# Optimization experiments

Hardware: AMD Instinct MI355X
Metric: run time of the kernel (lower is better)

## Reference

```python
import jax, jax.numpy as jnp
import numpy as np

B, S, M, H, P, T = 32, 400, 400, 200, 16, 4

def setup_inputs() -> dict:
    key = jax.random.key(0)
    ks = jax.random.split(key, 20)
    sc = 0.05
    inp = {
        'att': jax.random.normal(ks[0], (B, S, M), jnp.float32),
        'mod': jax.random.normal(ks[1], (B, S, M), jnp.float32),
        'mask': jnp.ones((B, S), jnp.float32),
        # LSTMCell: input 2*M, hidden H, gate order i,f,g,o
        'lstm_Wih': jax.random.normal(ks[2], (4 * H, 2 * M), jnp.float32) * sc,
        'lstm_Whh': jax.random.normal(ks[3], (4 * H, H), jnp.float32) * sc,
        'lstm_bih': jnp.zeros((4 * H,), jnp.float32),
        'lstm_bhh': jnp.zeros((4 * H,), jnp.float32),
    }
    for pfx, off in (('s', 4), ('e', 11)):
        inp[pfx + '_rW'] = jax.random.normal(ks[off + 0], (H, 2 * M + H), jnp.float32) * sc
        inp[pfx + '_W1'] = jax.random.normal(ks[off + 1], (P * H, M + H), jnp.float32) * sc
        inp[pfx + '_b1'] = jnp.zeros((P * H,), jnp.float32)
        inp[pfx + '_W2'] = jax.random.normal(ks[off + 2], (P * H, H), jnp.float32) * sc
        inp[pfx + '_b2'] = jnp.zeros((P * H,), jnp.float32)
        inp[pfx + '_W3'] = jax.random.normal(ks[off + 3], (P, 2 * H), jnp.float32) * sc
        inp[pfx + '_b3'] = jnp.zeros((P,), jnp.float32)
    return inp

def _gather(mod, idx):
    # mod:[B,S,M], idx:[B] -> [B,M]
    return jnp.take_along_axis(mod, idx[:, None, None], axis=1)[:, 0, :]

def _lstm_cell(x, h, c, Wih, Whh, bih, bhh):
    g = x @ Wih.T + bih + h @ Whh.T + bhh  # [B,4H]
    i, f, gg, o = jnp.split(g, 4, axis=1)
    c2 = jax.nn.sigmoid(f) * c + jax.nn.sigmoid(i) * jnp.tanh(gg)
    h2 = jax.nn.sigmoid(o) * jnp.tanh(c2)
    return h2, c2

def _hmn(mod, h, us, ue, mask, rW, W1, b1, W2, b2, W3, b3):
    r = jnp.tanh(jnp.concatenate([h, us, ue], 1) @ rW.T)  # [B,H]
    x = jnp.concatenate([mod, jnp.broadcast_to(r[:, None, :], (B, S, H))], 2)  # [B,S,M+H]
    m1 = (x @ W1.T + b1).reshape(B, S, P, H).max(2)   # maxout 1
    m2 = (m1 @ W2.T + b2).reshape(B, S, P, H).max(2)  # maxout 2
    logits = (jnp.concatenate([m1, m2], 2) @ W3.T + b3).max(2)  # [B,S]
    logits = jnp.where(mask > 0, logits, -1e30)
    return jax.nn.log_softmax(logits, axis=1)

def reference(att, mod, mask, lstm_Wih, lstm_Whh, lstm_bih, lstm_bhh,
              s_rW, s_W1, s_b1, s_W2, s_b2, s_W3, s_b3,
              e_rW, e_W1, e_b1, e_W2, e_b2, e_W3, e_b3):
    s_prev = jnp.zeros((B,), jnp.int32)
    e_prev = jnp.sum(mask, 1).astype(jnp.int32) - 1
    h = jnp.zeros((B, H), mod.dtype)
    c = jnp.zeros((B, H), mod.dtype)
    log_p1s, log_p2s = [], []
    for _ in range(T):
        u_s = _gather(mod, s_prev)
        u_e = _gather(mod, e_prev)
        h, c = _lstm_cell(jnp.concatenate([u_s, u_e], 1), h, c,
                          lstm_Wih, lstm_Whh, lstm_bih, lstm_bhh)
        lp1 = _hmn(mod, h, u_s, u_e, mask, s_rW, s_W1, s_b1, s_W2, s_b2, s_W3, s_b3)
        s_prev = jnp.argmax(lp1, axis=1).astype(jnp.int32)
        u_s = _gather(mod, s_prev)
        lp2 = _hmn(mod, h, u_s, u_e, mask, e_rW, e_W1, e_b1, e_W2, e_b2, e_W3, e_b3)
        e_prev = jnp.argmax(lp2, axis=1).astype(jnp.int32)
        log_p1s.append(lp1)
        log_p2s.append(lp2)
    return jnp.stack(log_p1s, 1), jnp.stack(log_p2s, 1)  # each [B,T,S]
```

## Files before the change

kernel.cpp:

```cpp
#include <hip/hip_runtime.h>
#include <math.h>

#define NB 32
#define NS 400
#define NM 400
#define NH 200
#define NP 16
#define NT 4
#define NBS (NB*NS)
#define NPH (NP*NH)
#define NPH2 3328
#define NJT 13
#define NX  (2*NM)
#define NG  (4*NH)
#define NR  (2*NM+NH)
#define K1  1216
#define K2  608

typedef __attribute__((ext_vector_type(8))) short short8v;
typedef __attribute__((ext_vector_type(4))) float f32x4;
typedef __attribute__((ext_vector_type(4))) unsigned short us4;
typedef unsigned short ushort;

__device__ __forceinline__ float sigf(float x){ return 1.0f/(1.0f+expf(-x)); }

__device__ __forceinline__ ushort f2bf(float x){
  union{float f; unsigned u;} v; v.f=x;
  unsigned r = v.u + 0x7fffu + ((v.u>>16)&1u);
  return (ushort)(r>>16);
}
__device__ __forceinline__ float bf2f(ushort u){
  union{float f; unsigned v;} x; x.v = ((unsigned)u)<<16; return x.f;
}
__device__ __forceinline__ float wave_sum(float v){
  #pragma unroll
  for (int o=32;o>0;o>>=1) v += __shfl_xor(v, o);
  return v;
}

__global__ __launch_bounds__(256) void init_kernel(const float* __restrict__ mask,
    float* __restrict__ h, float* __restrict__ c,
    int* __restrict__ sprev, int* __restrict__ eprev){
  int b = blockIdx.x, tid = threadIdx.x;
  __shared__ float red[256];
  float s = 0.f;
  for (int i=tid;i<NS;i+=256) s += mask[(size_t)b*NS+i];
  red[tid]=s; __syncthreads();
  for (int st=128;st>0;st>>=1){ if(tid<st) red[tid]+=red[tid+st]; __syncthreads(); }
  if (tid==0){ sprev[b]=0; eprev[b]=(int)red[0]-1; }
  for (int i=tid;i<NH;i+=256){ h[(size_t)b*NH+i]=0.f; c[(size_t)b*NH+i]=0.f; }
}

__global__ __launch_bounds__(256) void conv_mod_k(const float* __restrict__ in, ushort* __restrict__ out){
  for (size_t i = (size_t)blockIdx.x*256+threadIdx.x; i < (size_t)NBS*K1; i += (size_t)gridDim.x*256){
    int r = (int)(i/K1), k = (int)(i%K1);
    ushort v = 0;
    if (k < 3*NM){
      float x = in[(size_t)r*NM + (k % NM)];
      ushort h = f2bf(x);
      v = (k < NM || k >= 2*NM) ? h : f2bf(x - bf2f(h));
    }
    out[i] = v;
  }
}
__global__ __launch_bounds__(256) void conv_w1_k(const float* __restrict__ in, ushort* __restrict__ out){
  for (size_t i = (size_t)blockIdx.x*256+threadIdx.x; i < (size_t)NPH2*K1; i += (size_t)gridDim.x*256){
    int jp = (int)(i/K1), k = (int)(i%K1);
    ushort v = 0;
    if (jp < NPH && k < 3*NM){
      int j = (jp&15)*NH + (jp>>4);
      float x = in[(size_t)j*(NM+NH) + (k % NM)];
      ushort h = f2bf(x);
      v = (k < 2*NM) ? h : f2bf(x - bf2f(h));
    }
    out[i] = v;
  }
}
__global__ __launch_bounds__(256) void conv_w2_k(const float* __restrict__ in, ushort* __restrict__ out){
  for (size_t i = (size_t)blockIdx.x*256+threadIdx.x; i < (size_t)NPH2*K2; i += (size_t)gridDim.x*256){
    int jp = (int)(i/K2), k = (int)(i%K2);
    ushort v = 0;
    if (jp < NPH && k < 3*NH){
      int j = (jp&15)*NH + (jp>>4);
      float x = in[(size_t)j*NH + (k % NH)];
      ushort h = f2bf(x);
      v = (k < 2*NH) ? h : f2bf(x - bf2f(h));
    }
    out[i] = v;
  }
}
__global__ __launch_bounds__(256) void conv_w1r_k(const float* __restrict__ in, float* __restrict__ out){
  for (size_t i = (size_t)blockIdx.x*256+threadIdx.x; i < (size_t)NH*NPH; i += (size_t)gridDim.x*256){
    int k = (int)(i/NPH), jp = (int)(i%NPH);
    int hh = jp>>4, p = jp&15, j = p*NH + hh;
    out[i] = in[(size_t)j*(NM+NH) + NM + k];
  }
}
__global__ __launch_bounds__(256) void permv_k(const float* __restrict__ in, float* __restrict__ out){
  int i = blockIdx.x*256+threadIdx.x;
  if (i < NPH) out[(i%NH)*NP + i/NH] = in[i];
  else if (i < NPH2) out[i] = 0.f;
}
__global__ __launch_bounds__(256) void pad_zero_k(ushort* __restrict__ p, int stride, int start, int width, int rows){
  for (size_t i = (size_t)blockIdx.x*256+threadIdx.x; i < (size_t)rows*width; i += (size_t)gridDim.x*256){
    int r = (int)(i/width), j = (int)(i%width);
    p[(size_t)r*stride + start + j] = 0;
  }
}

__global__ __launch_bounds__(256) void lstm_gates(const float* __restrict__ mod,
    const int* __restrict__ sprev, const int* __restrict__ eprev,
    const float* __restrict__ h,
    const float* __restrict__ Wih, const float* __restrict__ Whh,
    const float* __restrict__ bih, const float* __restrict__ bhh,
    float* __restrict__ gs){
  int b=blockIdx.x, tid=threadIdx.x;
  __shared__ float xs[NX+NH];
  const float* us = mod + ((size_t)b*NS + sprev[b])*NM;
  const float* ue = mod + ((size_t)b*NS + eprev[b])*NM;
  for (int i=tid;i<NM;i+=256){ xs[i]=us[i]; xs[NM+i]=ue[i]; }
  for (int i=tid;i<NH;i+=256) xs[NX+i]=h[(size_t)b*NH+i];
  __syncthreads();
  int w=tid>>6, lane=tid&63;
  int j = blockIdx.y*4 + w;
  const float* wih = Wih + (size_t)j*NX;
  const float* whh = Whh + (size_t)j*NH;
  float acc=0.f;
  for (int k=lane;k<NX;k+=64) acc += xs[k]*wih[k];
  for (int k=lane;k<NH;k+=64) acc += xs[NX+k]*whh[k];
  acc = wave_sum(acc);
  if (lane==0) gs[(size_t)b*NG+j] = acc + bih[j] + bhh[j];
}
__global__ __launch_bounds__(256) void lstm_update(const float* __restrict__ gs,
    float* __restrict__ h, float* __restrict__ c){
  int b=blockIdx.x, j=threadIdx.x;
  if (j<NH){
    float iv=gs[(size_t)b*NG+j], fv=gs[(size_t)b*NG+NH+j];
    float gv=gs[(size_t)b*NG+2*NH+j], ov=gs[(size_t)b*NG+3*NH+j];
    float c2 = sigf(fv)*c[(size_t)b*NH+j] + sigf(iv)*tanhf(gv);
    c[(size_t)b*NH+j]=c2;
    h[(size_t)b*NH+j]=sigf(ov)*tanhf(c2);
  }
}

__global__ __launch_bounds__(256) void r_kernel(const float* __restrict__ mod,
    const int* __restrict__ sprev, const int* __restrict__ eprev,
    const float* __restrict__ h, const float* __restrict__ rW,
    float* __restrict__ rbuf){
  int b=blockIdx.x, tid=threadIdx.x;
  __shared__ float zs[NR];
  const float* us = mod + ((size_t)b*NS + sprev[b])*NM;
  const float* ue = mod + ((size_t)b*NS + eprev[b])*NM;
  for (int i=tid;i<NH;i+=256) zs[i]=h[(size_t)b*NH+i];
  for (int i=tid;i<NM;i+=256){ zs[NH+i]=us[i]; zs[NH+NM+i]=ue[i]; }
  __syncthreads();
  int w=tid>>6, lane=tid&63;
  int j = blockIdx.y*4 + w;
  const float* wr = rW + (size_t)j*NR;
  float acc=0.f;
  for (int k=lane;k<NR;k+=64) acc += zs[k]*wr[k];
  acc = wave_sum(acc);
  if (lane==0) rbuf[(size_t)b*NH+j] = tanhf(acc);
}

__global__ __launch_bounds__(256) void prer_kernel(const float* __restrict__ rbuf,
    const float* __restrict__ W1rT, const float* __restrict__ b1p,
    float* __restrict__ prer){
  int b=blockIdx.x, tid=threadIdx.x;
  __shared__ float rs[NH];
  if (tid < NH) rs[tid] = rbuf[(size_t)b*NH+tid];
  __syncthreads();
  int jp = blockIdx.y*256 + tid;
  if (jp < NPH2){
    float acc = 0.f;
    if (jp < NPH){
      acc = b1p[jp];
      #pragma unroll 8
      for (int k=0;k<NH;k++) acc += rs[k]*W1rT[(size_t)k*NPH + jp];
    }
    prer[(size_t)b*NPH2 + jp] = acc;
  }
}

template<int MODE>
__global__ __launch_bounds__(512, 2) void gemm_fused(
    const ushort* __restrict__ A, const ushort* __restrict__ W,
    const float* __restrict__ bias, void* __restrict__ outp){
  constexpr int LDK = (MODE==1) ? K2 : K1;
  constexpr int NTI = LDK/32;
  __shared__ __align__(16) ushort As[4][256*32];
  __shared__ __align__(16) ushort Bs[4][256*32];
  __shared__ float biasLds[2][256];
  __shared__ float outT[256][16];
  const int tid = threadIdx.x;
  const int nwg = gridDim.x;
  const int q = nwg >> 3, r = nwg & 7;
  const int xcd = blockIdx.x & 7, sub = blockIdx.x >> 3;
  const int wkid = (xcd < r) ? (xcd*(q+1) + sub) : (r*(q+1) + (xcd-r)*q + sub);
  const int i0 = (wkid / NJT) * 256, j0 = (wkid % NJT) * 256;
  const int b0 = i0/NS;
  if (MODE==0){
    if (tid<256) biasLds[0][tid] = bias[(size_t)b0*NPH2 + j0 + tid];
    else { int b1r=(i0+255)/NS; biasLds[1][tid-256] = bias[(size_t)b1r*NPH2 + j0 + (tid-256)]; }
  } else {
    if (tid<256) biasLds[0][tid] = bias[j0+tid];
  }
  const int w = tid>>6, l = tid&63;
  const int wr = w>>2, wc = w&3;
  const int fr = l&15, fk = l>>4;
  const int srow = w*32 + (l>>2);
  const int sslot = l&3;
  const int swzc = (sslot ^ ((srow>>1)&3))*8;
  const ushort* gA0 = A + (size_t)(i0+srow)*LDK + swzc;
  const ushort* gB0 = W + (size_t)(j0+srow)*LDK + swzc;
  const int ldsOff = srow*32 + sslot*8;
  auto stage = [&](int slot, int kt){
    const ushort* a = gA0 + kt*32;
    const ushort* b = gB0 + kt*32;
    __builtin_amdgcn_global_load_lds((const __attribute__((address_space(1))) void*)a,
        (__attribute__((address_space(3))) void*)(&As[slot][ldsOff]), 16, 0, 0);
    __builtin_amdgcn_global_load_lds((const __attribute__((address_space(1))) void*)(a + 16*LDK),
        (__attribute__((address_space(3))) void*)(&As[slot][ldsOff + 16*32]), 16, 0, 0);
    __builtin_amdgcn_global_load_lds((const __attribute__((address_space(1))) void*)b,
        (__attribute__((address_space(3))) void*)(&Bs[slot][ldsOff]), 16, 0, 0);
    __builtin_amdgcn_global_load_lds((const __attribute__((address_space(1))) void*)(b + 16*LDK),
        (__attribute__((address_space(3))) void*)(&Bs[slot][ldsOff + 16*32]), 16, 0, 0);
  };
  f32x4 acc[8][4] = {};
  stage(0,0); stage(1,1); stage(2,2);
  for (int t=0; t<NTI; t++){
    if (t+2 < NTI)      asm volatile("s_waitcnt vmcnt(8)\n\ts_barrier" ::: "memory");
    else if (t+1 < NTI) asm volatile("s_waitcnt vmcnt(4)\n\ts_barrier" ::: "memory");
    else                asm volatile("s_waitcnt vmcnt(0)\n\ts_barrier" ::: "memory");
    const int s = t&3;
    short8v a[8], b[4];
    #pragma unroll
    for (int m=0;m<8;m++){
      int row = wr*128 + m*16 + fr;
      a[m] = *(const short8v*)&As[s][row*32 + ((fk ^ ((row>>1)&3))*8)];
    }
    #pragma unroll
    for (int n=0;n<4;n++){
      int row = wc*64 + n*16 + fr;
      b[n] = *(const short8v*)&Bs[s][row*32 + ((fk ^ ((row>>1)&3))*8)];
    }
    if (t+3 < NTI) stage((t+3)&3, t+3);
    __builtin_amdgcn_s_setprio(1);
    #pragma unroll
    for (int m=0;m<8;m++)
      #pragma unroll
      for (int n=0;n<4;n++)
        acc[m][n] = __builtin_amdgcn_mfma_f32_16x16x32_bf16(a[m], b[n], acc[m][n], 0,0,0);
    __builtin_amdgcn_s_setprio(0);
  }
  __syncthreads();
  const int blim = (b0+1)*NS;
  #pragma unroll
  for (int m=0;m<8;m++){
    #pragma unroll
    for (int n=0;n<4;n++){
      int colL = wc*64 + n*16 + fr;
      int rbase = wr*128 + m*16 + fk*4;
      #pragma unroll
      for (int reg=0; reg<4; reg++){
        int rowL = rbase + reg;
        float bv = (MODE==0 && (i0+rowL) >= blim) ? biasLds[1][colL] : biasLds[0][colL];
        float v = acc[m][n][reg] + bv;
        v = fmaxf(v, __shfl_xor(v,1));
        v = fmaxf(v, __shfl_xor(v,2));
        v = fmaxf(v, __shfl_xor(v,4));
        v = fmaxf(v, __shfl_xor(v,8));
        if (fr==0) outT[rowL][wc*4+n] = v;
      }
    }
  }
  __syncthreads();
  {
    int rowL = tid>>1;
    int hloc0 = (tid&1)*8;
    int hg0 = (j0>>4) + hloc0;
    if (hg0 < NH){
      int absrow = i0 + rowL;
      float v[8];
      #pragma unroll
      for (int qq=0;qq<8;qq++) v[qq] = outT[rowL][hloc0+qq];
      if (MODE==0){
        ushort* o = (ushort*)outp + (size_t)absrow*K2 + hg0;
        ushort hi[8], lo[8];
        #pragma unroll
        for (int qq=0;qq<8;qq++){ hi[qq]=f2bf(v[qq]); lo[qq]=f2bf(v[qq]-bf2f(hi[qq])); }
        *(us4*)(o)        = (us4){hi[0],hi[1],hi[2],hi[3]};
        *(us4*)(o+4)      = (us4){hi[4],hi[5],hi[6],hi[7]};
        *(us4*)(o+NH)     = (us4){lo[0],lo[1],lo[2],lo[3]};
        *(us4*)(o+NH+4)   = (us4){lo[4],lo[5],lo[6],lo[7]};
        *(us4*)(o+2*NH)   = (us4){hi[0],hi[1],hi[2],hi[3]};
        *(us4*)(o+2*NH+4) = (us4){hi[4],hi[5],hi[6],hi[7]};
      } else {
        float* o = (float*)outp + (size_t)absrow*NH + hg0;
        *(f32x4*)o     = (f32x4){v[0],v[1],v[2],v[3]};
        *(f32x4*)(o+4) = (f32x4){v[4],v[5],v[6],v[7]};
      }
    }
  }
}

__global__ __launch_bounds__(256) void logits_main(const ushort* __restrict__ m1e,
    const float* __restrict__ m2, const float* __restrict__ W3, const float* __restrict__ b3,
    const float* __restrict__ mask, float* __restrict__ lg){
  int b=blockIdx.x;
  int s=blockIdx.y*256+threadIdx.x;
  if (s >= NS) return;
  const ushort* a = m1e + (size_t)(b*NS+s)*K2;
  const float4* d = (const float4*)(m2 + (size_t)(b*NS+s)*NH);
  float acc[NP];
  #pragma unroll
  for (int p=0;p<NP;p++) acc[p]=b3[p];
  for (int k=0;k<NH/4;k++){
    us4 hv = *(const us4*)(a + 4*k);
    us4 lv = *(const us4*)(a + NH + 4*k);
    float4 dv = d[k];
    float a0=bf2f(hv.x)+bf2f(lv.x), a1=bf2f(hv.y)+bf2f(lv.y);
    float a2=bf2f(hv.z)+bf2f(lv.z), a3=bf2f(hv.w)+bf2f(lv.w);
    #pragma unroll
    for (int p=0;p<NP;p++){
      const float* wp = W3 + p*(2*NH) + 4*k;
      acc[p] += a0*wp[0]+a1*wp[1]+a2*wp[2]+a3*wp[3];
      const float* w2 = wp + NH;
      acc[p] += dv.x*w2[0]+dv.y*w2[1]+dv.z*w2[2]+dv.w*w2[3];
    }
  }
  float best=acc[0];
  #pragma unroll
  for (int p=1;p<NP;p++) best=fmaxf(best,acc[p]);
  lg[(size_t)b*NS+s] = (mask[(size_t)b*NS+s] > 0.f) ? best : -1e30f;
}

__global__ __launch_bounds__(256) void logits_fin(const float* __restrict__ lg,
    float* __restrict__ out, int t, int* __restrict__ prevIdx){
  int b=blockIdx.x, tid=threadIdx.x;
  __shared__ float rv[256]; __shared__ int ri[256]; __shared__ float sv[256];
  float bv=-INFINITY; int bi=NS;
  for (int s=tid;s<NS;s+=256){ float v=lg[(size_t)b*NS+s]; if (v>bv){bv=v;bi=s;} }
  rv[tid]=bv; ri[tid]=bi; __syncthreads();
  for (int st=128;st>0;st>>=1){
    if (tid<st){
      float v2=rv[tid+st]; int i2=ri[tid+st];
      if (v2>rv[tid] || (v2==rv[tid] && i2<ri[tid])){ rv[tid]=v2; ri[tid]=i2; }
    }
    __syncthreads();
  }
  float mx = rv[0];
  float ps=0.f;
  for (int s=tid;s<NS;s+=256) ps += expf(lg[(size_t)b*NS+s]-mx);
  sv[tid]=ps; __syncthreads();
  for (int st=128;st>0;st>>=1){ if (tid<st) sv[tid]+=sv[tid+st]; __syncthreads(); }
  float lse = mx + logf(sv[0]);
  for (int s=tid;s<NS;s+=256) out[((size_t)b*NT + t)*NS + s] = lg[(size_t)b*NS+s]-lse;
  if (tid==0) prevIdx[b]=ri[0];
}

extern "C" void kernel_launch(void* const* d_in, const int* in_sizes, int n_in,
                              void* d_out, int out_size, void* d_ws, size_t ws_size,
                              hipStream_t stream){
  const float* mod  = (const float*)d_in[1];
  const float* mask = (const float*)d_in[2];
  const float* Wih  = (const float*)d_in[3];
  const float* Whh  = (const float*)d_in[4];
  const float* bih  = (const float*)d_in[5];
  const float* bhh  = (const float*)d_in[6];
  const float* rW[2] = {(const float*)d_in[7],  (const float*)d_in[14]};
  const float* W1[2] = {(const float*)d_in[8],  (const float*)d_in[15]};
  const float* b1[2] = {(const float*)d_in[9],  (const float*)d_in[16]};
  const float* W2[2] = {(const float*)d_in[10], (const float*)d_in[17]};
  const float* b2[2] = {(const float*)d_in[11], (const float*)d_in[18]};
  const float* W3[2] = {(const float*)d_in[12], (const float*)d_in[19]};
  const float* b3[2] = {(const float*)d_in[13], (const float*)d_in[20]};
  float* out[2];
  out[0] = (float*)d_out;
  out[1] = out[0] + (size_t)NB*NT*NS;

  float* wsf = (float*)d_ws;
  size_t off = 0;
  auto carve = [&](size_t n)->size_t{ size_t o=off; off += (n + 63) & ~(size_t)63; return o; };
  float* hbuf   = wsf + carve((size_t)NB*NH);
  float* cbuf   = wsf + carve((size_t)NB*NH);
  float* prer   = wsf + carve((size_t)NB*NPH2);
  int*   sprev  = (int*)(wsf + carve(128));
  int*   eprev  = sprev + 32;
  float* m2f    = wsf + carve((size_t)NBS*NH);
  float* b2p[2] = {wsf + carve(NPH2), wsf + carve(NPH2)};
  float* b1p[2] = {wsf + carve(NPH2), wsf + carve(NPH2)};
  float* rbuf   = wsf + carve((size_t)NB*NH);
  float* gsbuf  = wsf + carve((size_t)NB*NG);
  float* lgbuf  = wsf + carve((size_t)NB*NS);
  float* W1rT[2]= {wsf + carve((size_t)NH*NPH), wsf + carve((size_t)NH*NPH)};
  ushort* modExp   = (ushort*)(wsf + carve((size_t)NBS*K1/2));
  ushort* W1exp[2] = {(ushort*)(wsf + carve((size_t)NPH2*K1/2)),
                      (ushort*)(wsf + carve((size_t)NPH2*K1/2))};
  ushort* W2exp[2] = {(ushort*)(wsf + carve((size_t)NPH2*K2/2)),
                      (ushort*)(wsf + carve((size_t)NPH2*K2/2))};
  ushort* m1exp    = (ushort*)(wsf + carve((size_t)NBS*K2/2));

  init_kernel<<<NB, 256, 0, stream>>>(mask, hbuf, cbuf, sprev, eprev);
  conv_mod_k<<<2048, 256, 0, stream>>>(mod, modExp);
  pad_zero_k<<<128, 256, 0, stream>>>(m1exp, K2, 3*NH, K2-3*NH, NBS);
  for (int net=0; net<2; net++){
    conv_w1_k<<<1024, 256, 0, stream>>>(W1[net], W1exp[net]);
    conv_w2_k<<<512, 256, 0, stream>>>(W2[net], W2exp[net]);
    conv_w1r_k<<<1024, 256, 0, stream>>>(W1[net], W1rT[net]);
    permv_k<<<(NPH2+255)/256, 256, 0, stream>>>(b2[net], b2p[net]);
    permv_k<<<(NPH2+255)/256, 256, 0, stream>>>(b1[net], b1p[net]);
  }

  const int GFULL = (NBS/256) * NJT;
  for (int t=0; t<NT; t++){
    lstm_gates<<<dim3(NB, NG/4), 256, 0, stream>>>(mod, sprev, eprev, hbuf,
                                                   Wih, Whh, bih, bhh, gsbuf);
    lstm_update<<<NB, 256, 0, stream>>>(gsbuf, hbuf, cbuf);
    for (int net=0; net<2; net++){
      r_kernel<<<dim3(NB, NH/4), 256, 0, stream>>>(mod, sprev, eprev, hbuf, rW[net], rbuf);
      prer_kernel<<<dim3(NB, NPH2/256), 256, 0, stream>>>(rbuf, W1rT[net], b1p[net], prer);
      gemm_fused<0><<<GFULL, 512, 0, stream>>>(modExp, W1exp[net], prer, (void*)m1exp);
      gemm_fused<1><<<GFULL, 512, 0, stream>>>(m1exp, W2exp[net], b2p[net], (void*)m2f);
      logits_main<<<dim3(NB, 2), 256, 0, stream>>>(m1exp, m2f, W3[net], b3[net], mask, lgbuf);
      logits_fin<<<NB, 256, 0, stream>>>(lgbuf, out[net], t, net==0 ? sprev : eprev);
    }
  }
}
```

Measured before the change: 2.968 ms.

## Parallelize logits kernel across pieces with LDS-staged W3 and shuffle max

The logits kernel now gives each thread one maxout piece instead of all 16. Sixteen lanes share one sequence row and combine their results with a warp-shuffle max. W3 is staged in shared memory with padding, and the grid grows from 64 blocks to 800. The goal is to remove the under-occupied, serial per-thread loop over pieces. The cost is that each row's activations are read redundantly by 16 lanes, and every block reloads W3 into shared memory.

```diff
diff --git a/kernel.cpp b/kernel.cpp
--- a/kernel.cpp
+++ b/kernel.cpp
@@ -307,32 +307,35 @@
 __global__ __launch_bounds__(256) void logits_main(const ushort* __restrict__ m1e,
     const float* __restrict__ m2, const float* __restrict__ W3, const float* __restrict__ b3,
     const float* __restrict__ mask, float* __restrict__ lg){
-  int b=blockIdx.x;
-  int s=blockIdx.y*256+threadIdx.x;
-  if (s >= NS) return;
+  __shared__ float w3s[NP][2*NH+1];
+  int b = blockIdx.x, tid = threadIdx.x;
+  for (int e = tid; e < NP*2*NH; e += 256)
+    w3s[e/(2*NH)][e%(2*NH)] = W3[e];
+  __syncthreads();
+  int sl = tid >> 4, p = tid & 15;
+  int s = blockIdx.y*16 + sl;
   const ushort* a = m1e + (size_t)(b*NS+s)*K2;
   const float4* d = (const float4*)(m2 + (size_t)(b*NS+s)*NH);
-  float acc[NP];
-  #pragma unroll
-  for (int p=0;p<NP;p++) acc[p]=b3[p];
+  float acc = b3[p];
+  const float* wp = &w3s[p][0];
   for (int k=0;k<NH/4;k++){
     us4 hv = *(const us4*)(a + 4*k);
     us4 lv = *(const us4*)(a + NH + 4*k);
     float4 dv = d[k];
     float a0=bf2f(hv.x)+bf2f(lv.x), a1=bf2f(hv.y)+bf2f(lv.y);
     float a2=bf2f(hv.z)+bf2f(lv.z), a3=bf2f(hv.w)+bf2f(lv.w);
-    #pragma unroll
-    for (int p=0;p<NP;p++){
-      const float* wp = W3 + p*(2*NH) + 4*k;
-      acc[p] += a0*wp[0]+a1*wp[1]+a2*wp[2]+a3*wp[3];
-      const float* w2 = wp + NH;
-      acc[p] += dv.x*w2[0]+dv.y*w2[1]+dv.z*w2[2]+dv.w*w2[3];
-    }
-  }
-  float best=acc[0];
-  #pragma unroll
-  for (int p=1;p<NP;p++) best=fmaxf(best,acc[p]);
-  lg[(size_t)b*NS+s] = (mask[(size_t)b*NS+s] > 0.f) ? best : -1e30f;
+    const float* w = wp + 4*k;
+    acc += a0*w[0]+a1*w[1]+a2*w[2]+a3*w[3];
+    const float* w2 = w + NH;
+    acc += dv.x*w2[0]+dv.y*w2[1]+dv.z*w2[2]+dv.w*w2[3];
+  }
+  float best = acc;
+  best = fmaxf(best, __shfl_xor(best,1));
+  best = fmaxf(best, __shfl_xor(best,2));
+  best = fmaxf(best, __shfl_xor(best,4));
+  best = fmaxf(best, __shfl_xor(best,8));
+  if (p == 0)
+    lg[(size_t)b*NS+s] = (mask[(size_t)b*NS+s] > 0.f) ? best : -1e30f;
 }
 
 __global__ __launch_bounds__(256) void logits_fin(const float* __restrict__ lg,
@@ -422,7 +425,7 @@
       prer_kernel<<<dim3(NB, NPH2/256), 256, 0, stream>>>(rbuf, W1rT[net], b1p[net], prer);
       gemm_fused<0><<<GFULL, 512, 0, stream>>>(modExp, W1exp[net], prer, (void*)m1exp);
       gemm_fused<1><<<GFULL, 512, 0, stream>>>(m1exp, W2exp[net], b2p[net], (void*)m2f);
-      logits_main<<<dim3(NB, 2), 256, 0, stream>>>(m1exp, m2f, W3[net], b3[net], mask, lgbuf);
+      logits_main<<<dim3(NB, NS/16), 256, 0, stream>>>(m1exp, m2f, W3[net], b3[net], mask, lgbuf);
       logits_fin<<<NB, 256, 0, stream>>>(lgbuf, out[net], t, net==0 ? sprev : eprev);
     }
   }
```

After: 2.601 ms (median of 2 runs). 1.14x faster.
